# Optimization experiments

Measured on AMD Instinct MI355X. Metric: run time of the kernel, lower is better.

## Reference

```python
import jax, jax.numpy as jnp
import numpy as np

BS, SL, D_IN, D_MODEL, H = 4, 128, 512, 512, 8
DP = D_MODEL // H


def setup_inputs() -> dict:
    key = jax.random.key(0)
    ks = jax.random.split(key, 12)
    s = 0.02
    inp = {
        "q": jax.random.normal(ks[0], (BS, SL, D_IN), jnp.float32),
        "k": jax.random.normal(ks[1], (BS, SL, D_IN), jnp.float32),
        "v": jax.random.normal(ks[2], (BS, SL, D_IN), jnp.float32),
    }
    j = jnp.arange(SL)
    # mask[t, jk] = 1.0 for the zero-padded slots jk > t in the shuffled sequence for step t
    mask2d = (j[None, :] > j[:, None]).astype(jnp.float32)  # (SL, SL)
    inp["mask"] = mask2d[None, :, None, None, :]            # (1, SL, 1, 1, SL)
    for i, n in enumerate(["wq", "wk", "wv", "dense"]):
        din = D_IN if n != "dense" else D_MODEL
        inp[n + "_w"] = jax.random.normal(ks[3 + 2 * i], (din, D_MODEL), jnp.float32) * s
        inp[n + "_b"] = jnp.zeros((D_MODEL,), jnp.float32)
    return inp


def _shuffle_idx(key, sl):
    # Row t of returned idx: random permutation of [0..t-1], then t, then t+1.. (padding slots).
    u = jax.random.uniform(key, (sl, sl))
    j = jnp.arange(sl)
    t = j[:, None]
    sort_keys = jnp.where(j[None, :] < t, u, j[None, :].astype(jnp.float32) + 2.0)
    return jnp.argsort(sort_keys, axis=-1)  # (sl, sl) int32


def _split_heads_shuffled(x, idx, valid):
    # x: (bs, sl, d) -> (bs, sl, H, sl, DP); padding slots (j > t) zeroed like torch plc_holder
    bs, sl, d = x.shape
    xt = x[:, idx, :] * valid[None, :, :, None]  # (bs, sl, sl, d)
    xt = xt.reshape(bs, sl, sl, H, DP)
    return xt.transpose(0, 1, 3, 2, 4)


def reference(q, k, v, mask, wq_w, wq_b, wk_w, wk_b, wv_w, wv_b, dense_w, dense_b):
    bs, sl, _ = q.shape
    j = jnp.arange(sl)
    valid = (j[None, :] <= j[:, None]).astype(q.dtype)  # (sl, sl)
    pkey = jax.random.key(42)
    idx_q = _shuffle_idx(jax.random.fold_in(pkey, 0), sl)
    idx_k = _shuffle_idx(jax.random.fold_in(pkey, 1), sl)
    idx_v = _shuffle_idx(jax.random.fold_in(pkey, 2), sl)

    qp = q @ wq_w + wq_b
    kp = k @ wk_w + wk_b
    vp = v @ wv_w + wv_b

    qh = _split_heads_shuffled(qp, idx_q, valid)  # (bs, sl, H, sl, DP)
    kh = _split_heads_shuffled(kp, idx_k, valid)
    vh = _split_heads_shuffled(vp, idx_v, valid)

    logits = jnp.einsum('bthqd,bthkd->bthqk', qh, kh) / jnp.sqrt(jnp.float32(DP))
    logits = logits + mask * (-1e9)
    attn = jax.nn.softmax(logits, axis=-1)          # (bs, sl, H, sl, sl)
    ctx = jnp.einsum('bthqk,bthkd->bthqd', attn, vh)  # (bs, sl, H, sl, DP)

    ctx = ctx.transpose(0, 1, 3, 2, 4).reshape(bs, sl, sl, H * DP)
    eff = ctx[:, j, j, :]                           # query row t of step t (the token itself)
    out = eff @ dense_w + dense_b                   # (bs, sl, d_model); dropout p=0 -> identity
    return (out, attn)
```

## Files before the change

### kernel.cpp

```cpp
#include <hip/hip_runtime.h>
#include <stdint.h>


#define BSZ 4
#define SLEN 128
#define DMODEL 512
#define NHEAD 8
#define HDIM 64

__device__ __forceinline__ uint32_t rotl32(uint32_t v, int d) {
  return (v << d) | (v >> (32 - d));
}

__device__ __forceinline__ void tf2x32(uint32_t k0, uint32_t k1, uint32_t x0,
                                       uint32_t x1, uint32_t& y0, uint32_t& y1) {
  uint32_t ks2 = k0 ^ k1 ^ 0x1BD11BDAu;
  x0 += k0; x1 += k1;
#define TF_R(r) { x0 += x1; x1 = rotl32(x1, (r)); x1 ^= x0; }
  TF_R(13) TF_R(15) TF_R(26) TF_R(6)
  x0 += k1;  x1 += ks2 + 1u;
  TF_R(17) TF_R(29) TF_R(16) TF_R(24)
  x0 += ks2; x1 += k0 + 2u;
  TF_R(13) TF_R(15) TF_R(26) TF_R(6)
  x0 += k0;  x1 += k1 + 3u;
  TF_R(17) TF_R(29) TF_R(16) TF_R(24)
  x0 += k1;  x1 += ks2 + 4u;
  TF_R(13) TF_R(15) TF_R(26) TF_R(6)
  x0 += ks2; x1 += k0 + 5u;
#undef TF_R
  y0 = x0; y1 = x1;
}

__device__ __forceinline__ uint16_t f32_to_bf16(float v) {
  uint32_t x = __float_as_uint(v);
  return (uint16_t)((x + 0x7FFFu + ((x >> 16) & 1u)) >> 16);
}
__device__ __forceinline__ float bf16_to_f32(uint16_t b) {
  return __uint_as_float(((uint32_t)b) << 16);
}

__global__ __launch_bounds__(128) void idx_kernel(int* __restrict__ idx) {
  const int m = blockIdx.x;
  const int t = blockIdx.y;
  const int j = threadIdx.x;
  __shared__ float u[SLEN];
  uint32_t fk0, fk1;
  tf2x32(0u, 42u, 0u, (uint32_t)m, fk0, fk1);
  const int flat = t * SLEN + j;
  uint32_t y0, y1;
  tf2x32(fk0, fk1, 0u, (uint32_t)flat, y0, y1);
  uint32_t bits = y0 ^ y1;
  float uu = __uint_as_float((bits >> 9) | 0x3f800000u) - 1.0f;
  u[j] = uu;
  __syncthreads();
  int* row = idx + (m * SLEN + t) * SLEN;
  if (j >= t) {
    row[j] = j;
  } else {
    int rank = 0;
    for (int i = 0; i < t; ++i) {
      float ui = u[i];
      rank += ((ui < uu) || (ui == uu && i < j)) ? 1 : 0;
    }
    row[rank] = j;
  }
}

__device__ __forceinline__ void gemm512_body(const float* __restrict__ A,
                                             const float* __restrict__ W,
                                             const float* __restrict__ bias,
                                             float* __restrict__ C,
                                             float* As , float* Ws ) {
  const int tid = threadIdx.x;
  const int tx = tid & 15, ty = tid >> 4;
  const int row0 = blockIdx.y * 64, col0 = blockIdx.x * 64;
  const int lr = tid >> 2, lc = (tid & 3) << 2;
  const int wr = tid >> 4, wc = (tid & 15) << 2;
  float acc[4][4] = {};
  for (int k0 = 0; k0 < 512; k0 += 16) {
    float4 av = *(const float4*)(A + (size_t)(row0 + lr) * 512 + k0 + lc);
    float4 wv = *(const float4*)(W + (size_t)(k0 + wr) * 512 + col0 + wc);
    As[lr * 17 + lc + 0] = av.x; As[lr * 17 + lc + 1] = av.y;
    As[lr * 17 + lc + 2] = av.z; As[lr * 17 + lc + 3] = av.w;
    *(float4*)(Ws + wr * 64 + wc) = wv;
    __syncthreads();
#pragma unroll
    for (int kk = 0; kk < 16; ++kk) {
      float a[4], b[4];
#pragma unroll
      for (int i = 0; i < 4; ++i) a[i] = As[(ty * 4 + i) * 17 + kk];
#pragma unroll
      for (int jj = 0; jj < 4; ++jj) b[jj] = Ws[kk * 64 + tx * 4 + jj];
#pragma unroll
      for (int i = 0; i < 4; ++i)
#pragma unroll
        for (int jj = 0; jj < 4; ++jj) acc[i][jj] += a[i] * b[jj];
    }
    __syncthreads();
  }
#pragma unroll
  for (int i = 0; i < 4; ++i) {
    int r = row0 + ty * 4 + i, c = col0 + tx * 4;
    float4 o;
    o.x = acc[i][0] + bias[c + 0];
    o.y = acc[i][1] + bias[c + 1];
    o.z = acc[i][2] + bias[c + 2];
    o.w = acc[i][3] + bias[c + 3];
    *(float4*)(C + (size_t)r * 512 + c) = o;
  }
}

__global__ __launch_bounds__(256) void proj_kernel(
    const float* __restrict__ q, const float* __restrict__ k, const float* __restrict__ v,
    const float* __restrict__ wq, const float* __restrict__ wk, const float* __restrict__ wv,
    const float* __restrict__ bq, const float* __restrict__ bk, const float* __restrict__ bv,
    float* __restrict__ qp, float* __restrict__ kp, float* __restrict__ vp) {
  __shared__ float As[64 * 17];
  __shared__ float Ws[16 * 64];
  const float* A; const float* W; const float* B; float* C;
  if (blockIdx.z == 0)      { A = q; W = wq; B = bq; C = qp; }
  else if (blockIdx.z == 1) { A = k; W = wk; B = bk; C = kp; }
  else                      { A = v; W = wv; B = bv; C = vp; }
  gemm512_body(A, W, B, C, As, Ws);
}

__global__ __launch_bounds__(256) void dense_kernel(const float* __restrict__ A,
                                                    const float* __restrict__ W,
                                                    const float* __restrict__ B,
                                                    float* __restrict__ C) {
  __shared__ float As[64 * 17];
  __shared__ float Ws[16 * 64];
  gemm512_body(A, W, B, C, As, Ws);
}

__global__ __launch_bounds__(256) void sef_kernel(const float* __restrict__ qp,
                                                  const float* __restrict__ kp,
                                                  uint16_t* __restrict__ E,
                                                  float* __restrict__ Ft) {
  const int h = blockIdx.x, b = blockIdx.y;
  const int tid = threadIdx.x;
  __shared__ float qs[32 * 132];
  __shared__ float ks[32 * 132];
  __shared__ float redm[128 * 16];
  __shared__ float csum[128 * 16];
  __shared__ float m127s[SLEN];
  const float* qbase = qp + ((size_t)b * SLEN) * DMODEL + h * HDIM;
  const float* kbase = kp + ((size_t)b * SLEN) * DMODEL + h * HDIM;
  const int i0 = (tid >> 4) * 8, jg = tid & 15, j0 = jg * 8;
  float acc[8][8] = {};
  for (int d0 = 0; d0 < HDIM; d0 += 32) {
    __syncthreads();
    for (int it = 0; it < 4; ++it) {
      int flat = it * 256 + tid;
      int row = flat >> 3;
      int c4 = (flat & 7) << 2;
      float4 a = *(const float4*)(qbase + (size_t)row * DMODEL + d0 + c4);
      float4 bb = *(const float4*)(kbase + (size_t)row * DMODEL + d0 + c4);
      qs[(c4 + 0) * 132 + row] = a.x;  qs[(c4 + 1) * 132 + row] = a.y;
      qs[(c4 + 2) * 132 + row] = a.z;  qs[(c4 + 3) * 132 + row] = a.w;
      ks[(c4 + 0) * 132 + row] = bb.x; ks[(c4 + 1) * 132 + row] = bb.y;
      ks[(c4 + 2) * 132 + row] = bb.z; ks[(c4 + 3) * 132 + row] = bb.w;
    }
    __syncthreads();
    for (int d = 0; d < 32; ++d) {
      float4 qa = *(const float4*)(qs + d * 132 + i0);
      float4 qb = *(const float4*)(qs + d * 132 + i0 + 4);
      float4 ka = *(const float4*)(ks + d * 132 + j0);
      float4 kb = *(const float4*)(ks + d * 132 + j0 + 4);
      float a[8] = {qa.x, qa.y, qa.z, qa.w, qb.x, qb.y, qb.z, qb.w};
      float bb[8] = {ka.x, ka.y, ka.z, ka.w, kb.x, kb.y, kb.z, kb.w};
#pragma unroll
      for (int r = 0; r < 8; ++r)
#pragma unroll
        for (int c = 0; c < 8; ++c) acc[r][c] += a[r] * bb[c];
    }
  }
#pragma unroll
  for (int r = 0; r < 8; ++r) {
    float m = -3.402823466e38f;
#pragma unroll
    for (int c = 0; c < 8; ++c) {
      acc[r][c] *= 0.125f;
      m = fmaxf(m, acc[r][c]);
    }
    redm[(i0 + r) * 16 + jg] = m;
  }
  __syncthreads();
  if (tid < SLEN) {
    float m = redm[tid * 16];
#pragma unroll
    for (int g = 1; g < 16; ++g) m = fmaxf(m, redm[tid * 16 + g]);
    m127s[tid] = m;
  }
  __syncthreads();
  const int bh = b * NHEAD + h;
  uint16_t* Eb = E + (size_t)bh * SLEN * SLEN;
#pragma unroll
  for (int r = 0; r < 8; ++r) {
    const float m = m127s[i0 + r];
    float run = 0.f;
    ushort4 e0, e1;
    float ev;
    ev = __expf(acc[r][0] - m); e0.x = f32_to_bf16(ev); run += ev; acc[r][0] = run;
    ev = __expf(acc[r][1] - m); e0.y = f32_to_bf16(ev); run += ev; acc[r][1] = run;
    ev = __expf(acc[r][2] - m); e0.z = f32_to_bf16(ev); run += ev; acc[r][2] = run;
    ev = __expf(acc[r][3] - m); e0.w = f32_to_bf16(ev); run += ev; acc[r][3] = run;
    ev = __expf(acc[r][4] - m); e1.x = f32_to_bf16(ev); run += ev; acc[r][4] = run;
    ev = __expf(acc[r][5] - m); e1.y = f32_to_bf16(ev); run += ev; acc[r][5] = run;
    ev = __expf(acc[r][6] - m); e1.z = f32_to_bf16(ev); run += ev; acc[r][6] = run;
    ev = __expf(acc[r][7] - m); e1.w = f32_to_bf16(ev); run += ev; acc[r][7] = run;
    *(ushort4*)(Eb + (size_t)(i0 + r) * SLEN + j0) = e0;
    *(ushort4*)(Eb + (size_t)(i0 + r) * SLEN + j0 + 4) = e1;
    csum[(i0 + r) * 16 + jg] = run;
  }
  __syncthreads();
  float* Fb = Ft + (size_t)bh * SLEN * SLEN;
#pragma unroll
  for (int r = 0; r < 8; ++r) {
    float base = 0.f;
    for (int g = 0; g < 16; ++g) {
      if (g == jg) break;
      base += csum[(i0 + r) * 16 + g];
    }
#pragma unroll
    for (int c = 0; c < 8; ++c)
      Fb[(size_t)(j0 + c) * SLEN + (i0 + r)] = 1.0f / (base + acc[r][c]);
  }
}

__global__ __launch_bounds__(256) void attn_kernel(const uint16_t* __restrict__ E,
                                                   const float* __restrict__ Ft,
                                                   const int* __restrict__ idx,
                                                   const float* __restrict__ vp,
                                                   float* __restrict__ attn_out,
                                                   float* __restrict__ eff) {
  const int h = blockIdx.x;
  const int tg = blockIdx.y;
  const int b = blockIdx.z;
  const int tid = threadIdx.x;
  const int wave = tid >> 6, lane = tid & 63;
  const int half = lane >> 5, l32 = lane & 31;
  const int bh = b * NHEAD + h;
  __shared__ __align__(16) uint16_t Es[SLEN * SLEN];
  __shared__ int iqs[8][SLEN];
  __shared__ int iks[8][SLEN];
  __shared__ int ivs[8][SLEN];
  __shared__ float Fsl[8][SLEN];
  {
    const uint4* src = (const uint4*)(E + (size_t)bh * SLEN * SLEN);
    uint4* dst = (uint4*)Es;
#pragma unroll
    for (int i = 0; i < 8; ++i) dst[i * 256 + tid] = src[i * 256 + tid];
  }
  {
    const int t0 = tg * 8;
#pragma unroll
    for (int ii = 0; ii < 4; ++ii) {
      int i = ii * 256 + tid;
      int s = i >> 7, j = i & 127;
      int t = t0 + s;
      iqs[s][j] = idx[(0 * SLEN + t) * SLEN + j];
      iks[s][j] = idx[(1 * SLEN + t) * SLEN + j];
      ivs[s][j] = idx[(2 * SLEN + t) * SLEN + j];
      Fsl[s][j] = Ft[((size_t)bh * SLEN + t) * SLEN + j];
    }
  }
  __syncthreads();
  const int k0 = l32 * 4;
  const int d = (wave << 4) + (lane >> 2);
  const int kg = lane & 3;
  const float* vb = vp + (size_t)b * SLEN * DMODEL + h * HDIM + d;
  for (int s = 0; s < 8; ++s) {
    const int t = tg * 8 + s;
    const int ikA = iks[s][k0], ikB = iks[s][k0 + 1], ikC = iks[s][k0 + 2], ikD = iks[s][k0 + 3];
    float4 cm;
    cm.x = (k0 + 0 <= t) ? 1.f : 0.f;
    cm.y = (k0 + 1 <= t) ? 1.f : 0.f;
    cm.z = (k0 + 2 <= t) ? 1.f : 0.f;
    cm.w = (k0 + 3 <= t) ? 1.f : 0.f;
    const float inv = 1.0f / (float)(t + 1);
    float* obase = attn_out + ((size_t)((b * SLEN + t) * NHEAD + h)) * SLEN * SLEN;
#pragma unroll 2
    for (int q8 = wave * 2; q8 < SLEN; q8 += 8) {
      const int qe = q8 + half;
      float4 val;
      if (qe <= t) {
        const int iq = iqs[s][qe];
        const float f = Fsl[s][iq];
        const uint16_t* Er = Es + iq * SLEN;
        val.x = bf16_to_f32(Er[ikA]) * f * cm.x;
        val.y = bf16_to_f32(Er[ikB]) * f * cm.y;
        val.z = bf16_to_f32(Er[ikC]) * f * cm.z;
        val.w = bf16_to_f32(Er[ikD]) * f * cm.w;
      } else {
        val.x = inv * cm.x; val.y = inv * cm.y;
        val.z = inv * cm.z; val.w = inv * cm.w;
      }
      *(float4*)(obase + (size_t)qe * SLEN + k0) = val;
    }
    {
      const uint16_t* Et = Es + t * SLEN;
      float acc = 0.f;
      for (int k = kg; k <= t; k += 4)
        acc += bf16_to_f32(Et[iks[s][k]]) * vb[(size_t)ivs[s][k] * DMODEL];
      acc += __shfl_xor(acc, 1);
      acc += __shfl_xor(acc, 2);
      if (kg == 0)
        eff[((size_t)b * SLEN + t) * DMODEL + h * HDIM + d] = acc * Fsl[s][t];
    }
  }
}

extern "C" void kernel_launch(void* const* d_in, const int* in_sizes, int n_in,
                              void* d_out, int out_size, void* d_ws, size_t ws_size,
                              hipStream_t stream) {
  const float* q    = (const float*)d_in[0];
  const float* k    = (const float*)d_in[1];
  const float* v    = (const float*)d_in[2];
  const float* wq_w = (const float*)d_in[4];
  const float* wq_b = (const float*)d_in[5];
  const float* wk_w = (const float*)d_in[6];
  const float* wk_b = (const float*)d_in[7];
  const float* wv_w = (const float*)d_in[8];
  const float* wv_b = (const float*)d_in[9];
  const float* dw   = (const float*)d_in[10];
  const float* db   = (const float*)d_in[11];

  float* out  = (float*)d_out;
  float* attn = out + 262144;

  float* wsf = (float*)d_ws;
  uint16_t* E = (uint16_t*)wsf;
  int*   idx = (int*)(wsf + 262144);
  float* qp  = wsf + 311296;
  float* kp  = qp + 262144;
  float* vp  = kp + 262144;
  float* Ft  = vp + 262144;
  float* eff = Ft + 524288;
  (void)in_sizes; (void)n_in; (void)out_size; (void)ws_size;

  idx_kernel<<<dim3(3, 128, 1), 128, 0, stream>>>(idx);
  proj_kernel<<<dim3(8, 8, 3), 256, 0, stream>>>(q, k, v, wq_w, wk_w, wv_w,
                                                 wq_b, wk_b, wv_b, qp, kp, vp);
  sef_kernel<<<dim3(8, 4, 1), 256, 0, stream>>>(qp, kp, E, Ft);
  attn_kernel<<<dim3(8, 16, 4), 256, 0, stream>>>(E, Ft, idx, vp, attn, eff);
  dense_kernel<<<dim3(8, 8, 1), 256, 0, stream>>>(eff, dw, db, out);
}
```

Before: 421.5 us.

## Halve GEMM row tile, prefetch next K-slice into registers, nontemporal attn stores

The shared projection/dense GEMM body moves from 64x64 to 32x64 tiles, doubling the grid for more parallelism on the many CUs. It also prefetches the next K-slice from global memory into registers before the compute loop, overlapping loads with FMAs. Separately, the large attention-probability output is written with nontemporal stores to avoid polluting the cache. The trade-off is less data reuse per block in the GEMMs, and only half the threads load the A tile.

```diff
diff --git a/kernel.cpp b/kernel.cpp
--- a/kernel.cpp
+++ b/kernel.cpp
@@ -7,6 +7,8 @@
 #define DMODEL 512
 #define NHEAD 8
 #define HDIM 64
+
+typedef float f32x4_t __attribute__((ext_vector_type(4)));
 
 __device__ __forceinline__ uint32_t rotl32(uint32_t v, int d) {
   return (v << d) | (v >> (32 - d));
@@ -72,35 +74,44 @@
                                              float* __restrict__ C,
                                              float* As , float* Ws ) {
   const int tid = threadIdx.x;
-  const int tx = tid & 15, ty = tid >> 4;
-  const int row0 = blockIdx.y * 64, col0 = blockIdx.x * 64;
+  const int tx = tid & 15;
+  const int ty = tid >> 4;
+  const int row0 = blockIdx.y * 32, col0 = blockIdx.x * 64;
   const int lr = tid >> 2, lc = (tid & 3) << 2;
   const int wr = tid >> 4, wc = (tid & 15) << 2;
-  float acc[4][4] = {};
+  float acc[2][4] = {};
+  float4 av, wv;
+  if (tid < 128) av = *(const float4*)(A + (size_t)(row0 + lr) * 512 + lc);
+  wv = *(const float4*)(W + (size_t)wr * 512 + col0 + wc);
   for (int k0 = 0; k0 < 512; k0 += 16) {
-    float4 av = *(const float4*)(A + (size_t)(row0 + lr) * 512 + k0 + lc);
-    float4 wv = *(const float4*)(W + (size_t)(k0 + wr) * 512 + col0 + wc);
-    As[lr * 17 + lc + 0] = av.x; As[lr * 17 + lc + 1] = av.y;
-    As[lr * 17 + lc + 2] = av.z; As[lr * 17 + lc + 3] = av.w;
+    if (tid < 128) {
+      As[lr * 17 + lc + 0] = av.x; As[lr * 17 + lc + 1] = av.y;
+      As[lr * 17 + lc + 2] = av.z; As[lr * 17 + lc + 3] = av.w;
+    }
     *(float4*)(Ws + wr * 64 + wc) = wv;
     __syncthreads();
+    if (k0 + 16 < 512) {
+      if (tid < 128) av = *(const float4*)(A + (size_t)(row0 + lr) * 512 + k0 + 16 + lc);
+      wv = *(const float4*)(W + (size_t)(k0 + 16 + wr) * 512 + col0 + wc);
+    }
 #pragma unroll
     for (int kk = 0; kk < 16; ++kk) {
-      float a[4], b[4];
-#pragma unroll
-      for (int i = 0; i < 4; ++i) a[i] = As[(ty * 4 + i) * 17 + kk];
-#pragma unroll
-      for (int jj = 0; jj < 4; ++jj) b[jj] = Ws[kk * 64 + tx * 4 + jj];
-#pragma unroll
-      for (int i = 0; i < 4; ++i)
-#pragma unroll
-        for (int jj = 0; jj < 4; ++jj) acc[i][jj] += a[i] * b[jj];
+      float a0 = As[(ty * 2 + 0) * 17 + kk];
+      float a1 = As[(ty * 2 + 1) * 17 + kk];
+      float bvv[4];
+#pragma unroll
+      for (int jj = 0; jj < 4; ++jj) bvv[jj] = Ws[kk * 64 + tx * 4 + jj];
+#pragma unroll
+      for (int jj = 0; jj < 4; ++jj) {
+        acc[0][jj] += a0 * bvv[jj];
+        acc[1][jj] += a1 * bvv[jj];
+      }
     }
     __syncthreads();
   }
 #pragma unroll
-  for (int i = 0; i < 4; ++i) {
-    int r = row0 + ty * 4 + i, c = col0 + tx * 4;
+  for (int i = 0; i < 2; ++i) {
+    int r = row0 + ty * 2 + i, c = col0 + tx * 4;
     float4 o;
     o.x = acc[i][0] + bias[c + 0];
     o.y = acc[i][1] + bias[c + 1];
@@ -115,7 +126,7 @@
     const float* __restrict__ wq, const float* __restrict__ wk, const float* __restrict__ wv,
     const float* __restrict__ bq, const float* __restrict__ bk, const float* __restrict__ bv,
     float* __restrict__ qp, float* __restrict__ kp, float* __restrict__ vp) {
-  __shared__ float As[64 * 17];
+  __shared__ float As[32 * 17];
   __shared__ float Ws[16 * 64];
   const float* A; const float* W; const float* B; float* C;
   if (blockIdx.z == 0)      { A = q; W = wq; B = bq; C = qp; }
@@ -128,7 +139,7 @@
                                                     const float* __restrict__ W,
                                                     const float* __restrict__ B,
                                                     float* __restrict__ C) {
-  __shared__ float As[64 * 17];
+  __shared__ float As[32 * 17];
   __shared__ float Ws[16 * 64];
   gemm512_body(A, W, B, C, As, Ws);
 }
@@ -283,7 +294,7 @@
 #pragma unroll 2
     for (int q8 = wave * 2; q8 < SLEN; q8 += 8) {
       const int qe = q8 + half;
-      float4 val;
+      f32x4_t val;
       if (qe <= t) {
         const int iq = iqs[s][qe];
         const float f = Fsl[s][iq];
@@ -296,7 +307,7 @@
         val.x = inv * cm.x; val.y = inv * cm.y;
         val.z = inv * cm.z; val.w = inv * cm.w;
       }
-      *(float4*)(obase + (size_t)qe * SLEN + k0) = val;
+      __builtin_nontemporal_store(val, (f32x4_t*)(obase + (size_t)qe * SLEN + k0));
     }
     {
       const uint16_t* Et = Es + t * SLEN;
@@ -340,9 +351,9 @@
   (void)in_sizes; (void)n_in; (void)out_size; (void)ws_size;
 
   idx_kernel<<<dim3(3, 128, 1), 128, 0, stream>>>(idx);
-  proj_kernel<<<dim3(8, 8, 3), 256, 0, stream>>>(q, k, v, wq_w, wk_w, wv_w,
-                                                 wq_b, wk_b, wv_b, qp, kp, vp);
+  proj_kernel<<<dim3(8, 16, 3), 256, 0, stream>>>(q, k, v, wq_w, wk_w, wv_w,
+                                                  wq_b, wk_b, wv_b, qp, kp, vp);
   sef_kernel<<<dim3(8, 4, 1), 256, 0, stream>>>(qp, kp, E, Ft);
   attn_kernel<<<dim3(8, 16, 4), 256, 0, stream>>>(E, Ft, idx, vp, attn, eff);
-  dense_kernel<<<dim3(8, 8, 1), 256, 0, stream>>>(eff, dw, db, out);
-}
+  dense_kernel<<<dim3(8, 16, 1), 256, 0, stream>>>(eff, dw, db, out);
+}
```

Measured after the change: 385.0 us. 8.6% less time.
